# Kernel optimization log

Measured on AMD Instinct MI355X. Metric: run time of the kernel, lower is better.

The kernel has to match this reference:

```python
import jax, jax.numpy as jnp
import numpy as np

B, N, D = 8, 256, 128
LN_EPS = 1e-5


def setup_inputs() -> dict:
    key = jax.random.key(0)
    ks = jax.random.split(key, 12)
    s = 0.02
    return {
        "node_features": jax.random.normal(ks[0], (B, N, D), dtype=jnp.float32),
        "adjacency": jax.random.uniform(ks[1], (B, N, N), dtype=jnp.float32),
        "msg_w1": jax.random.normal(ks[2], (2 * D, D), dtype=jnp.float32) * s,
        "msg_b1": jnp.zeros((D,), jnp.float32),
        "msg_w2": jax.random.normal(ks[3], (D, D), dtype=jnp.float32) * s,
        "msg_b2": jnp.zeros((D,), jnp.float32),
        "upd_w1": jax.random.normal(ks[4], (2 * D, D), dtype=jnp.float32) * s,
        "upd_b1": jnp.zeros((D,), jnp.float32),
        "upd_w2": jax.random.normal(ks[5], (D, D), dtype=jnp.float32) * s,
        "upd_b2": jnp.zeros((D,), jnp.float32),
        "ln_g": jnp.ones((D,), jnp.float32),
        "ln_b": jnp.zeros((D,), jnp.float32),
    }


def reference(node_features, adjacency, msg_w1, msg_b1, msg_w2, msg_b2,
              upd_w1, upd_b1, upd_w2, upd_b2, ln_g, ln_b):
    d = node_features.shape[-1]
    n = node_features.shape[1]
    # Split the concat-then-matmul: cat(x_i, x_j) @ W1 == x_i @ W1[:d] + x_j @ W1[d:]
    hi = node_features @ msg_w1[:d]          # [B,N,D] (receiver i contribution)
    hj = node_features @ msg_w1[d:]          # [B,N,D] (sender j contribution)
    h = jax.nn.relu(hi[:, :, None, :] + hj[:, None, :, :] + msg_b1)  # [B,N,N,D]
    # Edge weights with the i==j pairs excluded (loop skips self-edges)
    a = adjacency * (1.0 - jnp.eye(n, dtype=adjacency.dtype))        # [B,N,N]
    # sum_j (h @ W2 + b2) * a_ij  ==  (sum_j h * a_ij) @ W2 + b2 * sum_j a_ij
    s = jnp.einsum('bijd,bij->bid', h, a)    # [B,N,D]
    agg = s @ msg_w2 + msg_b2 * jnp.sum(a, axis=-1, keepdims=True)   # [B,N,D]
    u = jnp.concatenate([node_features, agg], axis=-1)               # [B,N,2D]
    upd = jax.nn.relu(u @ upd_w1 + upd_b1) @ upd_w2 + upd_b2         # [B,N,D]
    res = node_features + upd
    mu = jnp.mean(res, axis=-1, keepdims=True)
    var = jnp.var(res, axis=-1, keepdims=True)
    return (res - mu) / jnp.sqrt(var + LN_EPS) * ln_g + ln_b
```

## Files before the change

### kernel.cpp

```cpp
#include <hip/hip_runtime.h>

#define BB 8
#define NN 256
#define DD 128
#define LN_EPS 1e-5f

__global__ __launch_bounds__(512) void k_proj(const float* __restrict__ x,
                                              const float* __restrict__ w1,
                                              const float* __restrict__ b1,
                                              float* __restrict__ hi,
                                              float* __restrict__ hjb) {
    __shared__ float xs[8][DD];
    __shared__ float part_a[4][8][DD];
    __shared__ float part_b[4][8][DD];
    const int row0 = blockIdx.x * 8;
    const int tid  = threadIdx.x;
    #pragma unroll
    for (int t = tid; t < 8 * DD; t += 512)
        xs[t >> 7][t & 127] = x[row0 * DD + t];
    __syncthreads();

    const int dp = tid & 127;
    const int kg = tid >> 7;
    const int kb = kg * 32;

    float acc_a[8] = {}, acc_b[8] = {};
    #pragma unroll
    for (int k4 = 0; k4 < 8; ++k4) {
        const int k0 = kb + k4 * 4;
        float wa[4], wb[4];
        #pragma unroll
        for (int q = 0; q < 4; ++q) {
            wa[q] = w1[(k0 + q) * DD + dp];
            wb[q] = w1[(DD + k0 + q) * DD + dp];
        }
        #pragma unroll
        for (int r = 0; r < 8; ++r) {
            const float4 xv = *(const float4*)&xs[r][k0];
            acc_a[r] = fmaf(xv.x, wa[0], acc_a[r]);
            acc_a[r] = fmaf(xv.y, wa[1], acc_a[r]);
            acc_a[r] = fmaf(xv.z, wa[2], acc_a[r]);
            acc_a[r] = fmaf(xv.w, wa[3], acc_a[r]);
            acc_b[r] = fmaf(xv.x, wb[0], acc_b[r]);
            acc_b[r] = fmaf(xv.y, wb[1], acc_b[r]);
            acc_b[r] = fmaf(xv.z, wb[2], acc_b[r]);
            acc_b[r] = fmaf(xv.w, wb[3], acc_b[r]);
        }
    }
    #pragma unroll
    for (int r = 0; r < 8; ++r) {
        part_a[kg][r][dp] = acc_a[r];
        part_b[kg][r][dp] = acc_b[r];
    }
    __syncthreads();
    #pragma unroll
    for (int m = 0; m < 2; ++m) {
        int idx = tid + m * 512;
        int r = idx >> 7, d = idx & 127;
        float sa = part_a[0][r][d] + part_a[1][r][d] + part_a[2][r][d] + part_a[3][r][d];
        float sb = part_b[0][r][d] + part_b[1][r][d] + part_b[2][r][d] + part_b[3][r][d];
        hi [(row0 + r) * DD + d] = sa;
        hjb[(row0 + r) * DD + d] = sb + b1[d];
    }
}

__global__ __launch_bounds__(256) void k_pair(const float* __restrict__ adj,
                                              const float* __restrict__ hi,
                                              const float* __restrict__ hjb,
                                              float* __restrict__ s_base,
                                              float* __restrict__ asum_base) {
    __shared__ float a_t[16][64];
    __shared__ float hjs[64][DD];
    const int bid = blockIdx.x;
    const int jq  = bid & 3;
    const int ig  = (bid >> 2) & 15;
    const int b   = bid >> 6;
    const int i0  = ig * 16;
    const int j0  = jq * 64;
    const int tid = threadIdx.x;

    float* __restrict__ s_out = s_base + (size_t)jq * BB * NN * DD;
    float* __restrict__ asum  = asum_base + jq * BB * NN;

    #pragma unroll
    for (int t = 0; t < 4; ++t) {
        int idx = tid + t * 256;
        int il = idx >> 6, jj = idx & 63;
        int i_g = i0 + il, j_g = j0 + jj;
        float av = adj[(b * NN + i_g) * NN + j_g];
        a_t[il][jj] = (j_g == i_g) ? 0.f : av;
    }
    {
        const float4* src = (const float4*)(hjb + (b * NN + j0) * DD);
        #pragma unroll
        for (int t = 0; t < 8; ++t) {
            int idx = tid + t * 256;
            ((float4*)hjs)[idx] = src[idx];
        }
    }
    __syncthreads();

    {
        int il = tid >> 4, l = tid & 15;
        float s = a_t[il][l] + a_t[il][l + 16] + a_t[il][l + 32] + a_t[il][l + 48];
        #pragma unroll
        for (int m = 8; m; m >>= 1) s += __shfl_xor(s, m, 16);
        if (l == 0) asum[b * NN + i0 + il] = s;
    }

    const int dq = tid & 31;
    const int rg = tid >> 5;
    const int r0 = rg * 2, r1 = r0 + 1;
    const float4 hi0 = *(const float4*)&hi[(b * NN + i0 + r0) * DD + dq * 4];
    const float4 hi1 = *(const float4*)&hi[(b * NN + i0 + r1) * DD + dq * 4];
    float4 acc0 = {0.f, 0.f, 0.f, 0.f}, acc1 = {0.f, 0.f, 0.f, 0.f};

    #pragma unroll 4
    for (int jj = 0; jj < 64; ++jj) {
        const float4 hv = *(const float4*)&hjs[jj][dq * 4];
        const float a0 = a_t[r0][jj];
        const float a1 = a_t[r1][jj];
        acc0.x = fmaf(fmaxf(hi0.x + hv.x, 0.f), a0, acc0.x);
        acc0.y = fmaf(fmaxf(hi0.y + hv.y, 0.f), a0, acc0.y);
        acc0.z = fmaf(fmaxf(hi0.z + hv.z, 0.f), a0, acc0.z);
        acc0.w = fmaf(fmaxf(hi0.w + hv.w, 0.f), a0, acc0.w);
        acc1.x = fmaf(fmaxf(hi1.x + hv.x, 0.f), a1, acc1.x);
        acc1.y = fmaf(fmaxf(hi1.y + hv.y, 0.f), a1, acc1.y);
        acc1.z = fmaf(fmaxf(hi1.z + hv.z, 0.f), a1, acc1.z);
        acc1.w = fmaf(fmaxf(hi1.w + hv.w, 0.f), a1, acc1.w);
    }
    *(float4*)&s_out[(b * NN + i0 + r0) * DD + dq * 4] = acc0;
    *(float4*)&s_out[(b * NN + i0 + r1) * DD + dq * 4] = acc1;
}

__global__ __launch_bounds__(512) void k_tail(const float* __restrict__ x,
                                              const float* __restrict__ s_base,
                                              const float* __restrict__ asum_base,
                                              const float* __restrict__ w2,
                                              const float* __restrict__ b2,
                                              const float* __restrict__ w3,
                                              const float* __restrict__ b3,
                                              const float* __restrict__ w4,
                                              const float* __restrict__ b4,
                                              const float* __restrict__ g,
                                              const float* __restrict__ bet,
                                              float* __restrict__ out) {
    __shared__ float part[4][8][DD];
    __shared__ float xs[8][DD];
    __shared__ float ss[8][DD];
    __shared__ float aggs[8][DD];
    __shared__ float u1s[8][DD];
    __shared__ float resS[8][DD];
    __shared__ float asum_s[8];

    const int row0 = blockIdx.x * 8;
    const int tid  = threadIdx.x;
    const int dp   = tid & 127;
    const int kg   = tid >> 7;
    const int kb   = kg * 32;
    const size_t BND = (size_t)BB * NN * DD;

    #pragma unroll
    for (int t = tid; t < 8 * DD; t += 512) {
        xs[t >> 7][t & 127] = x[row0 * DD + t];
        ss[t >> 7][t & 127] = s_base[row0 * DD + t]
                            + s_base[BND + row0 * DD + t]
                            + s_base[2 * BND + row0 * DD + t]
                            + s_base[3 * BND + row0 * DD + t];
    }
    if (tid < 8) {
        int r = row0 + tid;
        asum_s[tid] = asum_base[r] + asum_base[BB * NN + r]
                    + asum_base[2 * BB * NN + r] + asum_base[3 * BB * NN + r];
    }
    __syncthreads();

    {
        float acc[8] = {};
        #pragma unroll
        for (int k4 = 0; k4 < 8; ++k4) {
            const int k0 = kb + k4 * 4;
            float wv[4];
            #pragma unroll
            for (int q = 0; q < 4; ++q) wv[q] = w2[(k0 + q) * DD + dp];
            #pragma unroll
            for (int r = 0; r < 8; ++r) {
                const float4 sv = *(const float4*)&ss[r][k0];
                acc[r] = fmaf(sv.x, wv[0], acc[r]);
                acc[r] = fmaf(sv.y, wv[1], acc[r]);
                acc[r] = fmaf(sv.z, wv[2], acc[r]);
                acc[r] = fmaf(sv.w, wv[3], acc[r]);
            }
        }
        #pragma unroll
        for (int r = 0; r < 8; ++r) part[kg][r][dp] = acc[r];
    }
    __syncthreads();
    #pragma unroll
    for (int m = 0; m < 2; ++m) {
        int idx = tid + m * 512;
        int r = idx >> 7, d = idx & 127;
        aggs[r][d] = part[0][r][d] + part[1][r][d] + part[2][r][d] + part[3][r][d]
                   + b2[d] * asum_s[r];
    }
    __syncthreads();

    {
        float acc[8] = {};
        #pragma unroll
        for (int k4 = 0; k4 < 8; ++k4) {
            const int k0 = kb + k4 * 4;
            float wa[4], wb[4];
            #pragma unroll
            for (int q = 0; q < 4; ++q) {
                wa[q] = w3[(k0 + q) * DD + dp];
                wb[q] = w3[(DD + k0 + q) * DD + dp];
            }
            #pragma unroll
            for (int r = 0; r < 8; ++r) {
                const float4 xv = *(const float4*)&xs[r][k0];
                const float4 av = *(const float4*)&aggs[r][k0];
                acc[r] = fmaf(xv.x, wa[0], acc[r]);
                acc[r] = fmaf(xv.y, wa[1], acc[r]);
                acc[r] = fmaf(xv.z, wa[2], acc[r]);
                acc[r] = fmaf(xv.w, wa[3], acc[r]);
                acc[r] = fmaf(av.x, wb[0], acc[r]);
                acc[r] = fmaf(av.y, wb[1], acc[r]);
                acc[r] = fmaf(av.z, wb[2], acc[r]);
                acc[r] = fmaf(av.w, wb[3], acc[r]);
            }
        }
        #pragma unroll
        for (int r = 0; r < 8; ++r) part[kg][r][dp] = acc[r];
    }
    __syncthreads();
    #pragma unroll
    for (int m = 0; m < 2; ++m) {
        int idx = tid + m * 512;
        int r = idx >> 7, d = idx & 127;
        float v = part[0][r][d] + part[1][r][d] + part[2][r][d] + part[3][r][d] + b3[d];
        u1s[r][d] = fmaxf(v, 0.f);
    }
    __syncthreads();

    {
        float acc[8] = {};
        #pragma unroll
        for (int k4 = 0; k4 < 8; ++k4) {
            const int k0 = kb + k4 * 4;
            float wv[4];
            #pragma unroll
            for (int q = 0; q < 4; ++q) wv[q] = w4[(k0 + q) * DD + dp];
            #pragma unroll
            for (int r = 0; r < 8; ++r) {
                const float4 uv = *(const float4*)&u1s[r][k0];
                acc[r] = fmaf(uv.x, wv[0], acc[r]);
                acc[r] = fmaf(uv.y, wv[1], acc[r]);
                acc[r] = fmaf(uv.z, wv[2], acc[r]);
                acc[r] = fmaf(uv.w, wv[3], acc[r]);
            }
        }
        #pragma unroll
        for (int r = 0; r < 8; ++r) part[kg][r][dp] = acc[r];
    }
    __syncthreads();
    #pragma unroll
    for (int m = 0; m < 2; ++m) {
        int idx = tid + m * 512;
        int r = idx >> 7, d = idx & 127;
        resS[r][d] = xs[r][d]
                   + part[0][r][d] + part[1][r][d] + part[2][r][d] + part[3][r][d]
                   + b4[d];
    }
    __syncthreads();

    {
        const int r = tid >> 6, l = tid & 63;
        const float2 v = *(const float2*)&resS[r][l * 2];
        float s1 = v.x + v.y;
        float s2 = v.x * v.x + v.y * v.y;
        #pragma unroll
        for (int m = 32; m; m >>= 1) {
            s1 += __shfl_xor(s1, m);
            s2 += __shfl_xor(s2, m);
        }
        const float mu = s1 * (1.f / DD);
        const float rs = rsqrtf(s2 * (1.f / DD) - mu * mu + LN_EPS);
        const int d = l * 2;
        const float2 gv = *(const float2*)&g[d];
        const float2 bv = *(const float2*)&bet[d];
        float2 o;
        o.x = (v.x - mu) * rs * gv.x + bv.x;
        o.y = (v.y - mu) * rs * gv.y + bv.y;
        *(float2*)&out[(row0 + r) * DD + d] = o;
    }
}

extern "C" void kernel_launch(void* const* d_in, const int* in_sizes, int n_in,
                              void* d_out, int out_size, void* d_ws, size_t ws_size,
                              hipStream_t stream) {
    (void)in_sizes; (void)n_in; (void)out_size; (void)ws_size;
    const float* x      = (const float*)d_in[0];
    const float* adj    = (const float*)d_in[1];
    const float* msg_w1 = (const float*)d_in[2];
    const float* msg_b1 = (const float*)d_in[3];
    const float* msg_w2 = (const float*)d_in[4];
    const float* msg_b2 = (const float*)d_in[5];
    const float* upd_w1 = (const float*)d_in[6];
    const float* upd_b1 = (const float*)d_in[7];
    const float* upd_w2 = (const float*)d_in[8];
    const float* upd_b2 = (const float*)d_in[9];
    const float* ln_g   = (const float*)d_in[10];
    const float* ln_b   = (const float*)d_in[11];
    float* out = (float*)d_out;

    const size_t BND = (size_t)BB * NN * DD;
    float* ws     = (float*)d_ws;
    float* s4     = ws;
    float* asum4  = ws + 4 * BND;
    float* hi     = asum4 + 4 * BB * NN;
    float* hjb    = hi + BND;

    k_proj<<<dim3(BB * NN / 8), dim3(512), 0, stream>>>(x, msg_w1, msg_b1, hi, hjb);
    k_pair<<<dim3(512), dim3(256), 0, stream>>>(adj, hi, hjb, s4, asum4);
    k_tail<<<dim3(BB * NN / 8), dim3(512), 0, stream>>>(x, s4, asum4,
                                                        msg_w2, msg_b2,
                                                        upd_w1, upd_b1, upd_w2, upd_b2,
                                                        ln_g, ln_b, out);
}
```

Before: 30.16 us.

## Fuse pairwise aggregation with tail MLP and LayerNorm into one kernel

Merges the pairwise message-aggregation kernel and the tail kernel (W2 projection, update MLP, LayerNorm) into a single kernel. Each block now owns 8 receiver rows across all 256 senders, streaming hj tiles through shared memory, so the four partial-sum buffers in global memory and the extra launch go away. The tail GEMMs are re-tiled with 8 k-groups of 16 and each thread computing two output columns. The cost is a grid of only 256 blocks with a serial loop over j tiles, and heavier shared-memory aliasing with more syncs, which reduces parallelism.

```diff
diff --git a/kernel.cpp b/kernel.cpp
--- a/kernel.cpp
+++ b/kernel.cpp
@@ -64,219 +64,211 @@
     }
 }
 
-__global__ __launch_bounds__(256) void k_pair(const float* __restrict__ adj,
-                                              const float* __restrict__ hi,
-                                              const float* __restrict__ hjb,
-                                              float* __restrict__ s_base,
-                                              float* __restrict__ asum_base) {
-    __shared__ float a_t[16][64];
-    __shared__ float hjs[64][DD];
+__global__ __launch_bounds__(512) void k_fused(const float* __restrict__ adj,
+                                               const float* __restrict__ x,
+                                               const float* __restrict__ hi,
+                                               const float* __restrict__ hjb,
+                                               const float* __restrict__ w2,
+                                               const float* __restrict__ b2,
+                                               const float* __restrict__ w3,
+                                               const float* __restrict__ b3,
+                                               const float* __restrict__ w4,
+                                               const float* __restrict__ b4,
+                                               const float* __restrict__ g,
+                                               const float* __restrict__ bet,
+                                               float* __restrict__ out) {
+    __shared__ float smem[13320];
+    float* const a_t    = smem + 8192;
+    float* const xs     = smem + 10240;
+    float* const ssp    = smem + 11264;
+    float* const aggs   = smem + 12288;
+    float* const u1s    = smem + 8192;
+    float* const resS   = smem + 9216;
+    float* const part   = smem;
+    float* const asum_s = smem + 13312;
+
     const int bid = blockIdx.x;
-    const int jq  = bid & 3;
-    const int ig  = (bid >> 2) & 15;
-    const int b   = bid >> 6;
-    const int i0  = ig * 16;
-    const int j0  = jq * 64;
+    const int b   = bid >> 5;
+    const int i0  = (bid & 31) * 8;
     const int tid = threadIdx.x;
 
-    float* __restrict__ s_out = s_base + (size_t)jq * BB * NN * DD;
-    float* __restrict__ asum  = asum_base + jq * BB * NN;
-
     #pragma unroll
     for (int t = 0; t < 4; ++t) {
-        int idx = tid + t * 256;
-        int il = idx >> 6, jj = idx & 63;
-        int i_g = i0 + il, j_g = j0 + jj;
-        float av = adj[(b * NN + i_g) * NN + j_g];
-        a_t[il][jj] = (j_g == i_g) ? 0.f : av;
-    }
-    {
-        const float4* src = (const float4*)(hjb + (b * NN + j0) * DD);
-        #pragma unroll
-        for (int t = 0; t < 8; ++t) {
-            int idx = tid + t * 256;
-            ((float4*)hjs)[idx] = src[idx];
-        }
-    }
-    __syncthreads();
-
-    {
-        int il = tid >> 4, l = tid & 15;
-        float s = a_t[il][l] + a_t[il][l + 16] + a_t[il][l + 32] + a_t[il][l + 48];
-        #pragma unroll
-        for (int m = 8; m; m >>= 1) s += __shfl_xor(s, m, 16);
-        if (l == 0) asum[b * NN + i0 + il] = s;
-    }
-
-    const int dq = tid & 31;
-    const int rg = tid >> 5;
-    const int r0 = rg * 2, r1 = r0 + 1;
-    const float4 hi0 = *(const float4*)&hi[(b * NN + i0 + r0) * DD + dq * 4];
-    const float4 hi1 = *(const float4*)&hi[(b * NN + i0 + r1) * DD + dq * 4];
-    float4 acc0 = {0.f, 0.f, 0.f, 0.f}, acc1 = {0.f, 0.f, 0.f, 0.f};
-
-    #pragma unroll 4
-    for (int jj = 0; jj < 64; ++jj) {
-        const float4 hv = *(const float4*)&hjs[jj][dq * 4];
-        const float a0 = a_t[r0][jj];
-        const float a1 = a_t[r1][jj];
-        acc0.x = fmaf(fmaxf(hi0.x + hv.x, 0.f), a0, acc0.x);
-        acc0.y = fmaf(fmaxf(hi0.y + hv.y, 0.f), a0, acc0.y);
-        acc0.z = fmaf(fmaxf(hi0.z + hv.z, 0.f), a0, acc0.z);
-        acc0.w = fmaf(fmaxf(hi0.w + hv.w, 0.f), a0, acc0.w);
-        acc1.x = fmaf(fmaxf(hi1.x + hv.x, 0.f), a1, acc1.x);
-        acc1.y = fmaf(fmaxf(hi1.y + hv.y, 0.f), a1, acc1.y);
-        acc1.z = fmaf(fmaxf(hi1.z + hv.z, 0.f), a1, acc1.z);
-        acc1.w = fmaf(fmaxf(hi1.w + hv.w, 0.f), a1, acc1.w);
-    }
-    *(float4*)&s_out[(b * NN + i0 + r0) * DD + dq * 4] = acc0;
-    *(float4*)&s_out[(b * NN + i0 + r1) * DD + dq * 4] = acc1;
-}
-
-__global__ __launch_bounds__(512) void k_tail(const float* __restrict__ x,
-                                              const float* __restrict__ s_base,
-                                              const float* __restrict__ asum_base,
-                                              const float* __restrict__ w2,
-                                              const float* __restrict__ b2,
-                                              const float* __restrict__ w3,
-                                              const float* __restrict__ b3,
-                                              const float* __restrict__ w4,
-                                              const float* __restrict__ b4,
-                                              const float* __restrict__ g,
-                                              const float* __restrict__ bet,
-                                              float* __restrict__ out) {
-    __shared__ float part[4][8][DD];
-    __shared__ float xs[8][DD];
-    __shared__ float ss[8][DD];
-    __shared__ float aggs[8][DD];
-    __shared__ float u1s[8][DD];
-    __shared__ float resS[8][DD];
-    __shared__ float asum_s[8];
-
-    const int row0 = blockIdx.x * 8;
-    const int tid  = threadIdx.x;
-    const int dp   = tid & 127;
-    const int kg   = tid >> 7;
-    const int kb   = kg * 32;
-    const size_t BND = (size_t)BB * NN * DD;
-
-    #pragma unroll
-    for (int t = tid; t < 8 * DD; t += 512) {
-        xs[t >> 7][t & 127] = x[row0 * DD + t];
-        ss[t >> 7][t & 127] = s_base[row0 * DD + t]
-                            + s_base[BND + row0 * DD + t]
-                            + s_base[2 * BND + row0 * DD + t]
-                            + s_base[3 * BND + row0 * DD + t];
-    }
-    if (tid < 8) {
-        int r = row0 + tid;
-        asum_s[tid] = asum_base[r] + asum_base[BB * NN + r]
-                    + asum_base[2 * BB * NN + r] + asum_base[3 * BB * NN + r];
-    }
-    __syncthreads();
-
-    {
-        float acc[8] = {};
-        #pragma unroll
-        for (int k4 = 0; k4 < 8; ++k4) {
-            const int k0 = kb + k4 * 4;
-            float wv[4];
-            #pragma unroll
-            for (int q = 0; q < 4; ++q) wv[q] = w2[(k0 + q) * DD + dp];
-            #pragma unroll
-            for (int r = 0; r < 8; ++r) {
-                const float4 sv = *(const float4*)&ss[r][k0];
-                acc[r] = fmaf(sv.x, wv[0], acc[r]);
-                acc[r] = fmaf(sv.y, wv[1], acc[r]);
-                acc[r] = fmaf(sv.z, wv[2], acc[r]);
-                acc[r] = fmaf(sv.w, wv[3], acc[r]);
-            }
-        }
-        #pragma unroll
-        for (int r = 0; r < 8; ++r) part[kg][r][dp] = acc[r];
-    }
-    __syncthreads();
-    #pragma unroll
-    for (int m = 0; m < 2; ++m) {
-        int idx = tid + m * 512;
-        int r = idx >> 7, d = idx & 127;
-        aggs[r][d] = part[0][r][d] + part[1][r][d] + part[2][r][d] + part[3][r][d]
-                   + b2[d] * asum_s[r];
-    }
-    __syncthreads();
-
-    {
-        float acc[8] = {};
-        #pragma unroll
-        for (int k4 = 0; k4 < 8; ++k4) {
-            const int k0 = kb + k4 * 4;
-            float wa[4], wb[4];
+        int idx = tid + t * 512;
+        int il = idx >> 8, j = idx & 255;
+        int i_g = i0 + il;
+        float av = adj[((size_t)b * NN + i_g) * NN + j];
+        a_t[il * 256 + j] = (j == i_g) ? 0.f : av;
+    }
+    #pragma unroll
+    for (int t = 0; t < 2; ++t) {
+        int idx = tid + t * 512;
+        xs[idx] = x[((size_t)b * NN + i0) * DD + idx];
+    }
+    __syncthreads();
+
+    {
+        int w = tid >> 6, l = tid & 63;
+        float s = a_t[w * 256 + l] + a_t[w * 256 + l + 64]
+                + a_t[w * 256 + l + 128] + a_t[w * 256 + l + 192];
+        #pragma unroll
+        for (int m = 32; m; m >>= 1) s += __shfl_xor(s, m);
+        if (l == 0) asum_s[w] = s;
+    }
+
+    const int dq  = tid & 31;
+    const int rg  = tid >> 5;
+    const int row = rg & 7;
+    const int jh  = rg >> 3;
+    const float4 hi4 = *(const float4*)&hi[((size_t)b * NN + i0 + row) * DD + dq * 4];
+    float4 acc = {0.f, 0.f, 0.f, 0.f};
+
+    for (int jt = 0; jt < 4; ++jt) {
+        __syncthreads();
+        const float4* src = (const float4*)(hjb + ((size_t)b * NN + jt * 64) * DD);
+        float4* dst = (float4*)smem;
+        #pragma unroll
+        for (int t = 0; t < 4; ++t) dst[tid + t * 512] = src[tid + t * 512];
+        __syncthreads();
+        const int jb = jh * 32;
+        #pragma unroll 8
+        for (int jj = 0; jj < 32; ++jj) {
+            const int jl = jb + jj;
+            const float4 hv = *(const float4*)&smem[jl * 128 + dq * 4];
+            const float a = a_t[row * 256 + jt * 64 + jl];
+            acc.x = fmaf(fmaxf(hi4.x + hv.x, 0.f), a, acc.x);
+            acc.y = fmaf(fmaxf(hi4.y + hv.y, 0.f), a, acc.y);
+            acc.z = fmaf(fmaxf(hi4.z + hv.z, 0.f), a, acc.z);
+            acc.w = fmaf(fmaxf(hi4.w + hv.w, 0.f), a, acc.w);
+        }
+    }
+    __syncthreads();
+    *(float4*)&ssp[rg * 128 + dq * 4] = acc;
+    __syncthreads();
+    #pragma unroll
+    for (int t = 0; t < 2; ++t) {
+        int idx = tid + t * 512;
+        int r = idx >> 7, d = idx & 127;
+        ssp[r * 128 + d] += ssp[(r + 8) * 128 + d];
+    }
+    __syncthreads();
+
+    const int dp = tid & 63;
+    const int kg = tid >> 6;
+    const int kb = kg * 16;
+
+    {
+        float wv0[16], wv1[16];
+        #pragma unroll
+        for (int k = 0; k < 16; ++k) {
+            wv0[k] = w2[(kb + k) * DD + dp];
+            wv1[k] = w2[(kb + k) * DD + dp + 64];
+        }
+        #pragma unroll
+        for (int r = 0; r < 8; ++r) {
+            float a0 = 0.f, a1 = 0.f;
             #pragma unroll
             for (int q = 0; q < 4; ++q) {
-                wa[q] = w3[(k0 + q) * DD + dp];
-                wb[q] = w3[(DD + k0 + q) * DD + dp];
+                const float4 sv = *(const float4*)&ssp[r * 128 + kb + q * 4];
+                a0 = fmaf(sv.x, wv0[q*4+0], a0); a1 = fmaf(sv.x, wv1[q*4+0], a1);
+                a0 = fmaf(sv.y, wv0[q*4+1], a0); a1 = fmaf(sv.y, wv1[q*4+1], a1);
+                a0 = fmaf(sv.z, wv0[q*4+2], a0); a1 = fmaf(sv.z, wv1[q*4+2], a1);
+                a0 = fmaf(sv.w, wv0[q*4+3], a0); a1 = fmaf(sv.w, wv1[q*4+3], a1);
             }
+            part[kg * 1024 + r * 128 + dp]      = a0;
+            part[kg * 1024 + r * 128 + dp + 64] = a1;
+        }
+    }
+    __syncthreads();
+    #pragma unroll
+    for (int t = 0; t < 2; ++t) {
+        int idx = tid + t * 512;
+        int r = idx >> 7, d = idx & 127;
+        float s = part[r * 128 + d];
+        #pragma unroll
+        for (int w = 1; w < 8; ++w) s += part[w * 1024 + r * 128 + d];
+        aggs[r * 128 + d] = s + b2[d] * asum_s[r];
+    }
+    __syncthreads();
+
+    {
+        float wa0[16], wa1[16], wb0[16], wb1[16];
+        #pragma unroll
+        for (int k = 0; k < 16; ++k) {
+            wa0[k] = w3[(kb + k) * DD + dp];
+            wa1[k] = w3[(kb + k) * DD + dp + 64];
+            wb0[k] = w3[(DD + kb + k) * DD + dp];
+            wb1[k] = w3[(DD + kb + k) * DD + dp + 64];
+        }
+        #pragma unroll
+        for (int r = 0; r < 8; ++r) {
+            float a0 = 0.f, a1 = 0.f;
             #pragma unroll
-            for (int r = 0; r < 8; ++r) {
-                const float4 xv = *(const float4*)&xs[r][k0];
-                const float4 av = *(const float4*)&aggs[r][k0];
-                acc[r] = fmaf(xv.x, wa[0], acc[r]);
-                acc[r] = fmaf(xv.y, wa[1], acc[r]);
-                acc[r] = fmaf(xv.z, wa[2], acc[r]);
-                acc[r] = fmaf(xv.w, wa[3], acc[r]);
-                acc[r] = fmaf(av.x, wb[0], acc[r]);
-                acc[r] = fmaf(av.y, wb[1], acc[r]);
-                acc[r] = fmaf(av.z, wb[2], acc[r]);
-                acc[r] = fmaf(av.w, wb[3], acc[r]);
+            for (int q = 0; q < 4; ++q) {
+                const float4 xv = *(const float4*)&xs[r * 128 + kb + q * 4];
+                const float4 av = *(const float4*)&aggs[r * 128 + kb + q * 4];
+                a0 = fmaf(xv.x, wa0[q*4+0], a0); a1 = fmaf(xv.x, wa1[q*4+0], a1);
+                a0 = fmaf(xv.y, wa0[q*4+1], a0); a1 = fmaf(xv.y, wa1[q*4+1], a1);
+                a0 = fmaf(xv.z, wa0[q*4+2], a0); a1 = fmaf(xv.z, wa1[q*4+2], a1);
+                a0 = fmaf(xv.w, wa0[q*4+3], a0); a1 = fmaf(xv.w, wa1[q*4+3], a1);
+                a0 = fmaf(av.x, wb0[q*4+0], a0); a1 = fmaf(av.x, wb1[q*4+0], a1);
+                a0 = fmaf(av.y, wb0[q*4+1], a0); a1 = fmaf(av.y, wb1[q*4+1], a1);
+                a0 = fmaf(av.z, wb0[q*4+2], a0); a1 = fmaf(av.z, wb1[q*4+2], a1);
+                a0 = fmaf(av.w, wb0[q*4+3], a0); a1 = fmaf(av.w, wb1[q*4+3], a1);
             }
-        }
-        #pragma unroll
-        for (int r = 0; r < 8; ++r) part[kg][r][dp] = acc[r];
-    }
-    __syncthreads();
-    #pragma unroll
-    for (int m = 0; m < 2; ++m) {
-        int idx = tid + m * 512;
-        int r = idx >> 7, d = idx & 127;
-        float v = part[0][r][d] + part[1][r][d] + part[2][r][d] + part[3][r][d] + b3[d];
-        u1s[r][d] = fmaxf(v, 0.f);
-    }
-    __syncthreads();
-
-    {
-        float acc[8] = {};
-        #pragma unroll
-        for (int k4 = 0; k4 < 8; ++k4) {
-            const int k0 = kb + k4 * 4;
-            float wv[4];
+            part[kg * 1024 + r * 128 + dp]      = a0;
+            part[kg * 1024 + r * 128 + dp + 64] = a1;
+        }
+    }
+    __syncthreads();
+    #pragma unroll
+    for (int t = 0; t < 2; ++t) {
+        int idx = tid + t * 512;
+        int r = idx >> 7, d = idx & 127;
+        float s = part[r * 128 + d];
+        #pragma unroll
+        for (int w = 1; w < 8; ++w) s += part[w * 1024 + r * 128 + d];
+        u1s[r * 128 + d] = fmaxf(s + b3[d], 0.f);
+    }
+    __syncthreads();
+
+    {
+        float wv0[16], wv1[16];
+        #pragma unroll
+        for (int k = 0; k < 16; ++k) {
+            wv0[k] = w4[(kb + k) * DD + dp];
+            wv1[k] = w4[(kb + k) * DD + dp + 64];
+        }
+        #pragma unroll
+        for (int r = 0; r < 8; ++r) {
+            float a0 = 0.f, a1 = 0.f;
             #pragma unroll
-            for (int q = 0; q < 4; ++q) wv[q] = w4[(k0 + q) * DD + dp];
-            #pragma unroll
-            for (int r = 0; r < 8; ++r) {
-                const float4 uv = *(const float4*)&u1s[r][k0];
-                acc[r] = fmaf(uv.x, wv[0], acc[r]);
-                acc[r] = fmaf(uv.y, wv[1], acc[r]);
-                acc[r] = fmaf(uv.z, wv[2], acc[r]);
-                acc[r] = fmaf(uv.w, wv[3], acc[r]);
+            for (int q = 0; q < 4; ++q) {
+                const float4 uv = *(const float4*)&u1s[r * 128 + kb + q * 4];
+                a0 = fmaf(uv.x, wv0[q*4+0], a0); a1 = fmaf(uv.x, wv1[q*4+0], a1);
+                a0 = fmaf(uv.y, wv0[q*4+1], a0); a1 = fmaf(uv.y, wv1[q*4+1], a1);
+                a0 = fmaf(uv.z, wv0[q*4+2], a0); a1 = fmaf(uv.z, wv1[q*4+2], a1);
+                a0 = fmaf(uv.w, wv0[q*4+3], a0); a1 = fmaf(uv.w, wv1[q*4+3], a1);
             }
-        }
-        #pragma unroll
-        for (int r = 0; r < 8; ++r) part[kg][r][dp] = acc[r];
-    }
-    __syncthreads();
-    #pragma unroll
-    for (int m = 0; m < 2; ++m) {
-        int idx = tid + m * 512;
-        int r = idx >> 7, d = idx & 127;
-        resS[r][d] = xs[r][d]
-                   + part[0][r][d] + part[1][r][d] + part[2][r][d] + part[3][r][d]
-                   + b4[d];
+            part[kg * 1024 + r * 128 + dp]      = a0;
+            part[kg * 1024 + r * 128 + dp + 64] = a1;
+        }
+    }
+    __syncthreads();
+    #pragma unroll
+    for (int t = 0; t < 2; ++t) {
+        int idx = tid + t * 512;
+        int r = idx >> 7, d = idx & 127;
+        float s = part[r * 128 + d];
+        #pragma unroll
+        for (int w = 1; w < 8; ++w) s += part[w * 1024 + r * 128 + d];
+        resS[r * 128 + d] = xs[r * 128 + d] + s + b4[d];
     }
     __syncthreads();
 
     {
         const int r = tid >> 6, l = tid & 63;
-        const float2 v = *(const float2*)&resS[r][l * 2];
+        const float2 v = *(const float2*)&resS[r * 128 + l * 2];
         float s1 = v.x + v.y;
         float s2 = v.x * v.x + v.y * v.y;
         #pragma unroll
@@ -292,7 +284,7 @@
         float2 o;
         o.x = (v.x - mu) * rs * gv.x + bv.x;
         o.y = (v.y - mu) * rs * gv.y + bv.y;
-        *(float2*)&out[(row0 + r) * DD + d] = o;
+        *(float2*)&out[((size_t)b * NN + i0 + r) * DD + d] = o;
     }
 }
 
@@ -315,16 +307,13 @@
     float* out = (float*)d_out;
 
     const size_t BND = (size_t)BB * NN * DD;
-    float* ws     = (float*)d_ws;
-    float* s4     = ws;
-    float* asum4  = ws + 4 * BND;
-    float* hi     = asum4 + 4 * BB * NN;
-    float* hjb    = hi + BND;
+    float* ws  = (float*)d_ws;
+    float* hi  = ws;
+    float* hjb = ws + BND;
 
     k_proj<<<dim3(BB * NN / 8), dim3(512), 0, stream>>>(x, msg_w1, msg_b1, hi, hjb);
-    k_pair<<<dim3(512), dim3(256), 0, stream>>>(adj, hi, hjb, s4, asum4);
-    k_tail<<<dim3(BB * NN / 8), dim3(512), 0, stream>>>(x, s4, asum4,
-                                                        msg_w2, msg_b2,
-                                                        upd_w1, upd_b1, upd_w2, upd_b2,
-                                                        ln_g, ln_b, out);
+    k_fused<<<dim3(256), dim3(512), 0, stream>>>(adj, x, hi, hjb,
+                                                 msg_w2, msg_b2,
+                                                 upd_w1, upd_b1, upd_w2, upd_b2,
+                                                 ln_g, ln_b, out);
 }
```

Result: faster. 28.77 us (-4.6%).
